# Kernel tuning notes

Hardware: AMD Instinct MI355X
Metric: run time of the kernel (lower is better)

Reference implementation:

```python
import jax, jax.numpy as jnp
import numpy as np

N_NODES = 100000
N_EDGES = 1600000
D_IN = 128
D_HID = 128
D_OUT = 64


def setup_inputs() -> dict:
    key = jax.random.key(0)
    ks = jax.random.split(key, 8)
    x = jax.random.normal(ks[0], (N_NODES, D_IN), dtype=jnp.float32)
    edge_index = jax.random.randint(ks[1], (2, N_EDGES), 0, N_NODES, dtype=jnp.int64)
    s = 1.0 / np.sqrt(D_IN)
    W1l = jax.random.uniform(ks[2], (D_IN, D_HID), minval=-s, maxval=s, dtype=jnp.float32)
    W1r = jax.random.uniform(ks[3], (D_IN, D_HID), minval=-s, maxval=s, dtype=jnp.float32)
    b1 = jnp.zeros((D_HID,), dtype=jnp.float32)
    s2 = 1.0 / np.sqrt(D_HID)
    W2l = jax.random.uniform(ks[4], (D_HID, D_OUT), minval=-s2, maxval=s2, dtype=jnp.float32)
    W2r = jax.random.uniform(ks[5], (D_HID, D_OUT), minval=-s2, maxval=s2, dtype=jnp.float32)
    b2 = jnp.zeros((D_OUT,), dtype=jnp.float32)
    return {"x": x, "edge_index": edge_index, "drpt": 0,
            "W1l": W1l, "W1r": W1r, "b1": b1,
            "W2l": W2l, "W2r": W2r, "b2": b2}


def _mean_aggregate(x, src, dst, n_nodes):
    # gather source features along edges, scatter-mean to destinations
    gathered = x[src]                                   # [E, d]
    summed = jax.ops.segment_sum(gathered, dst, num_segments=n_nodes)  # [N, d]
    deg = jax.ops.segment_sum(jnp.ones((src.shape[0],), x.dtype), dst,
                              num_segments=n_nodes)     # [N]
    return summed / jnp.maximum(deg, 1.0)[:, None]


def _sage_conv(x, src, dst, Wl, Wr, b):
    # PyG SAGEConv (mean): out = agg @ Wl + b + x @ Wr
    agg = _mean_aggregate(x, src, dst, x.shape[0])
    return agg @ Wl + b + x @ Wr


def reference(x, edge_index, drpt, W1l, W1r, b1, W2l, W2r, b2):
    src, dst = edge_index[0], edge_index[1]
    h = _sage_conv(x, src, dst, W1l, W1r, b1)
    h = jax.nn.relu(h)
    # dropout is identity at inference (training=False)
    out = _sage_conv(h, src, dst, W2l, W2r, b2)
    return out
```

## Files before the change

kernel.cpp:

```cpp
#include <hip/hip_runtime.h>
#include <hip/hip_bf16.h>


#define N_NODES 100000
#define NGRP 6250
#define NBKT 391
#define ECHUNK 8192
#define BCAP 12288
#define NXB 12500
#define NWB 192

typedef __attribute__((ext_vector_type(8))) short short8v;
typedef __attribute__((ext_vector_type(4))) float f32x4;
typedef __attribute__((ext_vector_type(2))) uint u32x2;

__device__ inline ushort bf16_rne(float f) {
    union { float f; uint u; } c; c.f = f;
    uint u = c.u;
    return (ushort)((u + 0x7FFFu + ((u >> 16) & 1u)) >> 16);
}
__device__ inline float bf16_f(ushort h) {
    union { uint u; float f; } c; c.u = (uint)h << 16;
    return c.f;
}
__device__ inline unsigned char fp8_enc(float f) {
    union { float f; uint u; } c; c.f = f;
    uint u = c.u;
    uint s = (u >> 24) & 0x80u;
    uint a = u & 0x7FFFFFFFu;
    uint code;
    if (a >= 0x3C800000u) {
        uint r = a + 0x7FFFFu + ((a >> 20) & 1u);
        int e = (int)(r >> 23) - 120;
        uint mm = (r >> 20) & 7u;
        code = ((uint)e << 3) | mm;
        if (code > 0x7Eu) code = 0x7Eu;
    } else {
        code = (uint)(__uint_as_float(a) * 512.0f + 0.5f);
    }
    return (unsigned char)(s | code);
}

__device__ inline void gl_lds16(const void* g, void* l) {
    __builtin_amdgcn_global_load_lds(
        (const __attribute__((address_space(1))) uint*)g,
        (__attribute__((address_space(3))) uint*)l, 16, 0, 0);
}
__device__ inline uint lds_off(const void* p) {
    return (uint)(size_t)(const __attribute__((address_space(3))) char*)p;
}

__global__ __launch_bounds__(256) void k_prep(const float* __restrict__ x,
                                              const float* __restrict__ W1l,
                                              const float* __restrict__ W1r,
                                              const float* __restrict__ W2l,
                                              const float* __restrict__ W2r,
                                              const int* __restrict__ dst, int E,
                                              ushort* __restrict__ xh,
                                              unsigned char* __restrict__ xf8,
                                              ushort* __restrict__ BT1h,
                                              ushort* __restrict__ BT1l,
                                              ushort* __restrict__ BT2h,
                                              ushort* __restrict__ BT2l,
                                              int* __restrict__ bhist) {
    __shared__ int hsh[NBKT];
    const int b = blockIdx.x;
    if (b < NXB) {
        int i = (b * 256 + threadIdx.x) * 4;
        float4 v = *(const float4*)&x[i];
        ushort4 hh;
        hh.x = bf16_rne(v.x); hh.y = bf16_rne(v.y);
        hh.z = bf16_rne(v.z); hh.w = bf16_rne(v.w);
        *(ushort4*)&xh[i] = hh;
        uint f8 = (uint)fp8_enc(v.x) | ((uint)fp8_enc(v.y) << 8) |
                  ((uint)fp8_enc(v.z) << 16) | ((uint)fp8_enc(v.w) << 24);
        *(uint*)&xf8[i] = f8;
    } else if (b < NXB + NWB) {
        int id = (b - NXB) * 256 + threadIdx.x;
        if (id < 32768) {
            int n = id >> 8, k = id & 255;
            float v = (k < 128) ? W1l[k * 128 + n] : W1r[(k - 128) * 128 + n];
            ushort h = bf16_rne(v);
            BT1h[id] = h;
            BT1l[id] = bf16_rne(v - bf16_f(h));
        } else {
            int i = id - 32768;
            int n = i >> 7, k = i & 127;
            float v = (n < 64) ? W2l[k * 64 + n] : W2r[k * 64 + (n - 64)];
            ushort h = bf16_rne(v);
            BT2h[i] = h;
            BT2l[i] = bf16_rne(v - bf16_f(h));
        }
    } else {
        int bb = b - NXB - NWB;
        for (int i = threadIdx.x; i < NBKT; i += 256) hsh[i] = 0;
        __syncthreads();
        int b0 = bb * ECHUNK;
        for (int i = threadIdx.x; i < ECHUNK; i += 256) {
            int e = b0 + i;
            if (e < E) atomicAdd(&hsh[dst[e] >> 8], 1);
        }
        __syncthreads();
        for (int i = threadIdx.x; i < NBKT; i += 256)
            if (hsh[i]) atomicAdd(&bhist[i], hsh[i]);
    }
}

__global__ __launch_bounds__(512) void kA2_scan(const int* __restrict__ bhist,
                                                int* __restrict__ boff,
                                                int* __restrict__ bcur) {
    __shared__ int s[512];
    int t = threadIdx.x;
    s[t] = (t < NBKT) ? bhist[t] : 0;
    __syncthreads();
    for (int d = 1; d < 512; d <<= 1) {
        int v = (t >= d) ? s[t - d] : 0;
        __syncthreads();
        s[t] += v;
        __syncthreads();
    }
    if (t <= NBKT) {
        int e = (t == 0) ? 0 : s[t - 1];
        boff[t] = e;
        if (t < NBKT) bcur[t] = e;
    }
}

__global__ __launch_bounds__(256) void kA3_scatter(const int* __restrict__ src,
                                                   const int* __restrict__ dst,
                                                   int* __restrict__ bcur,
                                                   int* __restrict__ pairs, int E) {
    __shared__ int hist[NBKT];
    __shared__ int base[NBKT];
    __shared__ ushort rank[ECHUNK];
    for (int i = threadIdx.x; i < NBKT; i += 256) hist[i] = 0;
    __syncthreads();
    int b0 = blockIdx.x * ECHUNK;
    for (int i = threadIdx.x; i < ECHUNK; i += 256) {
        int e = b0 + i;
        if (e < E) rank[i] = (ushort)atomicAdd(&hist[dst[e] >> 8], 1);
    }
    __syncthreads();
    for (int i = threadIdx.x; i < NBKT; i += 256) {
        int c = hist[i];
        base[i] = c ? atomicAdd(&bcur[i], c) : 0;
    }
    __syncthreads();
    for (int i = threadIdx.x; i < ECHUNK; i += 256) {
        int e = b0 + i;
        if (e < E) {
            int d = dst[e];
            pairs[base[d >> 8] + rank[i]] = src[e] | ((d & 255) << 17);
        }
    }
}

__global__ __launch_bounds__(256) void kB_build(const int* __restrict__ pairs,
                                                const int* __restrict__ boff,
                                                int* __restrict__ csr,
                                                unsigned char* __restrict__ ldst,
                                                int* __restrict__ offsets,
                                                float* __restrict__ invdeg,
                                                int N, int E) {
    __shared__ int cntk[256];
    __shared__ int sck[256];
    __shared__ int cur[256];
    __shared__ int cntn[256];
    __shared__ int stage[BCAP];
    const int b = blockIdx.x;
    const int gbase = boff[b], gcount = boff[b + 1] - gbase;
    const int n0 = b << 8;
    const int t = threadIdx.x;

    cntk[t] = 0; cntn[t] = 0;
    __syncthreads();
    for (int i = t; i < gcount; i += 256) {
        int p = pairs[gbase + i];
        int dlow = (p >> 17) & 255;
        int key = (dlow & 0xF0) | ((p & 0x1FFFF) >> 13);
        atomicAdd(&cntk[key], 1);
        atomicAdd(&cntn[dlow], 1);
    }
    __syncthreads();
    sck[t] = cntk[t];
    __syncthreads();
    for (int d = 1; d < 256; d <<= 1) {
        int v = (t >= d) ? sck[t - d] : 0;
        __syncthreads();
        sck[t] += v;
        __syncthreads();
    }
    cur[t] = sck[t] - cntk[t];
    int node = n0 + t;
    if (node < N) {
        int gk = t & 0xF0;
        offsets[node] = gbase + sck[gk] - cntk[gk];
        invdeg[node] = 1.0f / fmaxf((float)cntn[t], 1.0f);
    }
    if (b == NBKT - 1 && t == 0) offsets[N] = E;
    __syncthreads();

    if (gcount <= BCAP) {
        for (int i = t; i < gcount; i += 256) {
            int p = pairs[gbase + i];
            int key = ((p >> 17) & 0xF0) | ((p & 0x1FFFF) >> 13);
            int pos = atomicAdd(&cur[key], 1);
            stage[pos] = p;
        }
        __syncthreads();
        for (int i = t; i < gcount; i += 256) {
            int p = stage[i];
            csr[gbase + i] = p & 0x1FFFF;
            ldst[gbase + i] = (unsigned char)((p >> 17) & 15);
        }
    } else {
        for (int i = t; i < gcount; i += 256) {
            int p = pairs[gbase + i];
            int key = ((p >> 17) & 0xF0) | ((p & 0x1FFFF) >> 13);
            int pos = atomicAdd(&cur[key], 1);
            csr[gbase + pos] = p & 0x1FFFF;
            ldst[gbase + pos] = (unsigned char)((p >> 17) & 15);
        }
    }
}

__global__ __launch_bounds__(64, 8) void k_agg1(const unsigned char* __restrict__ xf8,
                                                const int* __restrict__ csr,
                                                const unsigned char* __restrict__ ldst,
                                                const int* __restrict__ off,
                                                const float* __restrict__ invdeg,
                                                ushort* __restrict__ ah, int E) {
    __shared__ __align__(1024) char stg[4096];
    const int lane = threadIdx.x;
    const int g = blockIdx.x;
    const int gbase = off[g * 16], gend = off[g * 16 + 16];
    const int cnt = gend - gbase;
    const int m = lane & 15;
    const int e_meta = lane & 31;
    const int Emax = E - 1;
    const int esrc = lane >> 3;
    const int koff = ((lane & 7) ^ (esrc & 7)) << 4;

    f32x4 acc[8] = {};
    const int nch = (cnt + 31) >> 5;

    int pe = gbase + e_meta;
    int se = csr[(pe < Emax) ? pe : Emax];
    int lb = (pe < gend) ? (int)ldst[pe] : 255;

    const uint e7 = (lane >> 1) & 7;
    const uint bbase = lds_off(stg) + (uint)((lane >> 1) * 128 + (lane & 1) * 8);

    for (int ch = 0; ch < nch; ++ch) {
        #pragma unroll
        for (int c = 0; c < 4; ++c) {
            int rs = __shfl(se, c * 8 + esrc);
            gl_lds16((const char*)xf8 + (size_t)rs * 128 + koff, stg + c * 1024);
        }

        int p = gbase + (ch + 1) * 32 + e_meta;
        se = csr[(p < Emax) ? p : Emax];
        int lbn = (p < gend) ? (int)ldst[p] : 255;

        asm volatile("s_waitcnt vmcnt(0)" ::: "memory");
        __builtin_amdgcn_sched_barrier(0);

        unsigned long long av = 0ull;
        #pragma unroll
        for (int j = 0; j < 8; ++j) {
            int k = (lane >> 4) * 8 + j;
            int b = __shfl(lb, k);
            av |= (b == m) ? (0x38ull << (8 * j)) : 0ull;
        }

        #pragma unroll
        for (int th = 0; th < 2; ++th) {
            u32x2 tb[4];
            #pragma unroll
            for (int t4 = 0; t4 < 4; ++t4) {
                uint t = (uint)(th * 4 + t4);
                uint a1 = bbase + ((t ^ e7) << 4);
                asm volatile("ds_read_b64_tr_b8 %0, %1" : "=v"(tb[t4]) : "v"(a1));
            }
            asm volatile("s_waitcnt lgkmcnt(0)" ::: "memory");
            __builtin_amdgcn_sched_barrier(0);
            #pragma unroll
            for (int t4 = 0; t4 < 4; ++t4) {
                unsigned long long bv = ((unsigned long long)tb[t4].y << 32) | tb[t4].x;
                acc[th * 4 + t4] = __builtin_amdgcn_mfma_f32_16x16x32_fp8_fp8(
                    (long long)av, (long long)bv, acc[th * 4 + t4], 0, 0, 0);
            }
            __builtin_amdgcn_sched_barrier(0);
        }
        lb = lbn;
    }

    float idv[4];
    #pragma unroll
    for (int i = 0; i < 4; ++i) idv[i] = invdeg[g * 16 + (lane >> 4) * 4 + i];
    #pragma unroll
    for (int t = 0; t < 8; ++t) {
        #pragma unroll
        for (int i = 0; i < 4; ++i) {
            int node = g * 16 + (lane >> 4) * 4 + i;
            ah[(size_t)node * 128 + t * 16 + m] = bf16_rne(acc[t][i] * idv[i]);
        }
    }
}

__global__ __launch_bounds__(64, 8) void k_agg2(const ushort* __restrict__ hWl,
                                                const float* __restrict__ hWr,
                                                const int* __restrict__ csr,
                                                const unsigned char* __restrict__ ldst,
                                                const int* __restrict__ off,
                                                const float* __restrict__ invdeg,
                                                const float* __restrict__ b2,
                                                float* __restrict__ out, int E) {
    __shared__ __align__(1024) char stg[4096];
    const int lane = threadIdx.x;
    const int g = blockIdx.x;
    const int gbase = off[g * 16], gend = off[g * 16 + 16];
    const int cnt = gend - gbase;
    const int m = lane & 15;
    const int e_meta = lane & 31;
    const int Emax = E - 1;
    const int esrc = lane >> 3;
    const int koff = ((lane & 7) ^ ((esrc & 3) << 1)) << 4;

    f32x4 acc[4] = {};
    const int nch = (cnt + 31) >> 5;

    int pe = gbase + e_meta;
    int se = csr[(pe < Emax) ? pe : Emax];
    int lb = (pe < gend) ? (int)ldst[pe] : 255;

    const uint he = ((lane >> 1) & 1) ^ (((lane >> 2) & 3) << 1);
    const uint bbase = lds_off(stg) +
        (uint)(((lane >> 4) * 8 + ((lane >> 2) & 3)) * 128 + (lane & 1) * 8);

    for (int ch = 0; ch < nch; ++ch) {
        #pragma unroll
        for (int c = 0; c < 4; ++c) {
            int rs = __shfl(se, c * 8 + esrc);
            gl_lds16((const char*)hWl + (size_t)rs * 128 + koff, stg + c * 1024);
        }

        int p = gbase + (ch + 1) * 32 + e_meta;
        se = csr[(p < Emax) ? p : Emax];
        int lbn = (p < gend) ? (int)ldst[p] : 255;

        asm volatile("s_waitcnt vmcnt(0)" ::: "memory");
        __builtin_amdgcn_sched_barrier(0);

        uint au[4];
        #pragma unroll
        for (int jp = 0; jp < 4; ++jp) {
            int k0 = (lane >> 4) * 8 + jp * 2;
            int b0 = __shfl(lb, k0);
            int b1 = __shfl(lb, k0 + 1);
            au[jp] = ((b0 == m) ? 0x3F80u : 0u) | (((b1 == m) ? 0x3F80u : 0u) << 16);
        }
        union { uint u[4]; short8v v; } A_;
        A_.u[0] = au[0]; A_.u[1] = au[1]; A_.u[2] = au[2]; A_.u[3] = au[3];

        #pragma unroll
        for (int th = 0; th < 2; ++th) {
            u32x2 t1[2], t2[2];
            #pragma unroll
            for (int tt = 0; tt < 2; ++tt) {
                uint t = (uint)(th * 2 + tt);
                uint seg = (2u * t) ^ he;
                uint a1 = bbase + (seg << 4);
                uint a2 = a1 + 512;
                asm volatile("ds_read_b64_tr_b16 %0, %1" : "=v"(t1[tt]) : "v"(a1));
                asm volatile("ds_read_b64_tr_b16 %0, %1" : "=v"(t2[tt]) : "v"(a2));
            }
            asm volatile("s_waitcnt lgkmcnt(0)" ::: "memory");
            __builtin_amdgcn_sched_barrier(0);
            #pragma unroll
            for (int tt = 0; tt < 2; ++tt) {
                union { uint u[4]; short8v v; } B_;
                B_.u[0] = t1[tt].x; B_.u[1] = t1[tt].y;
                B_.u[2] = t2[tt].x; B_.u[3] = t2[tt].y;
                acc[th * 2 + tt] = __builtin_amdgcn_mfma_f32_16x16x32_bf16(
                    A_.v, B_.v, acc[th * 2 + tt], 0, 0, 0);
            }
            __builtin_amdgcn_sched_barrier(0);
        }
        lb = lbn;
    }

    float idv[4];
    #pragma unroll
    for (int i = 0; i < 4; ++i) idv[i] = invdeg[g * 16 + (lane >> 4) * 4 + i];
    #pragma unroll
    for (int t = 0; t < 4; ++t) {
        #pragma unroll
        for (int i = 0; i < 4; ++i) {
            int node = g * 16 + (lane >> 4) * 4 + i;
            size_t idx = (size_t)node * 64 + t * 16 + m;
            out[idx] = acc[t][i] * idv[i] + hWr[idx] + b2[t * 16 + m];
        }
    }
}

__global__ __launch_bounds__(256, 3) void k_mfma12(
    const ushort* __restrict__ Agg, const ushort* __restrict__ X,
    const ushort* __restrict__ B1h, const ushort* __restrict__ B1l,
    const ushort* __restrict__ B2h, const ushort* __restrict__ B2l,
    const float* __restrict__ b1,
    ushort* __restrict__ hWl, float* __restrict__ hWr, int M) {
    __shared__ ushort SM[24576];
    ushort* Bh  = SM;
    ushort* Bl  = SM + 4096;
    ushort* AhT = SM + 8192;

    const int tid = threadIdx.x;
    const int wid = tid >> 6, lane = tid & 63;
    const int wm = wid >> 1, wn = wid & 1;
    const int m0 = blockIdx.x * 128;
    const int rl = lane & 15, kq = lane >> 4;
    const int rq = kq;

    const int r0 = tid >> 2, r1 = r0 + 64;
    const int cq = tid & 3;
    int g0 = m0 + r0; if (g0 >= M) g0 = M - 1;
    int g1 = m0 + r1; if (g1 >= M) g1 = M - 1;
    const int q0 = (cq ^ ((r0 >> 1) & 3)) * 8;
    const int q1 = (cq ^ ((r1 >> 1) & 3)) * 8;
    const int ldso0 = r0 * 32 + cq * 8;
    const int ldso1 = r1 * 32 + cq * 8;

    int aof[4], bof[4];
    #pragma unroll
    for (int f = 0; f < 4; ++f) {
        int ra = wm * 64 + f * 16 + rl;
        int rb = wn * 64 + f * 16 + rl;
        aof[f] = ra * 32 + ((kq ^ ((ra >> 1) & 3)) << 3);
        bof[f] = rb * 32 + ((kq ^ ((rb >> 1) & 3)) << 3);
    }

    short8v pA0, pA1, pB0, pB1, pL0, pL1;
    {
        pA0 = *(const short8v*)&Agg[(size_t)g0 * 128 + q0];
        pA1 = *(const short8v*)&Agg[(size_t)g1 * 128 + q1];
        pB0 = *(const short8v*)&B1h[r0 * 256 + q0];
        pB1 = *(const short8v*)&B1h[r1 * 256 + q1];
        pL0 = *(const short8v*)&B1l[r0 * 256 + q0];
        pL1 = *(const short8v*)&B1l[r1 * 256 + q1];
    }
    f32x4 acc[4][4] = {};
    for (int kc = 0; kc < 8; ++kc) {
        *(short8v*)&AhT[ldso0] = pA0; *(short8v*)&AhT[ldso1] = pA1;
        *(short8v*)&Bh[ldso0]  = pB0; *(short8v*)&Bh[ldso1]  = pB1;
        *(short8v*)&Bl[ldso0]  = pL0; *(short8v*)&Bl[ldso1]  = pL1;
        __syncthreads();

        if (kc < 7) {
            int gk0 = (kc + 1) * 32 + q0;
            int gk1 = (kc + 1) * 32 + q1;
            const ushort* s0 = (kc + 1 >= 4) ? &X[(size_t)g0 * 128 + gk0 - 128]
                                             : &Agg[(size_t)g0 * 128 + gk0];
            const ushort* s1 = (kc + 1 >= 4) ? &X[(size_t)g1 * 128 + gk1 - 128]
                                             : &Agg[(size_t)g1 * 128 + gk1];
            pA0 = *(const short8v*)s0;
            pA1 = *(const short8v*)s1;
            pB0 = *(const short8v*)&B1h[r0 * 256 + gk0];
            pB1 = *(const short8v*)&B1h[r1 * 256 + gk1];
            pL0 = *(const short8v*)&B1l[r0 * 256 + gk0];
            pL1 = *(const short8v*)&B1l[r1 * 256 + gk1];
        }

        short8v a_h[4], b_h[4], b_l[4];
        #pragma unroll
        for (int f = 0; f < 4; ++f) {
            a_h[f] = *(const short8v*)&AhT[aof[f]];
            b_h[f] = *(const short8v*)&Bh[bof[f]];
            b_l[f] = *(const short8v*)&Bl[bof[f]];
        }
        #pragma unroll
        for (int mf = 0; mf < 4; ++mf)
            #pragma unroll
            for (int nf = 0; nf < 4; ++nf) {
                acc[mf][nf] = __builtin_amdgcn_mfma_f32_16x16x32_bf16(a_h[mf], b_h[nf], acc[mf][nf], 0, 0, 0);
                acc[mf][nf] = __builtin_amdgcn_mfma_f32_16x16x32_bf16(a_h[mf], b_l[nf], acc[mf][nf], 0, 0, 0);
            }
        __syncthreads();
    }

    short8v qB0, qB1, qL0, qL1;
    {
        qB0 = *(const short8v*)&B2h[r0 * 128 + q0];
        qB1 = *(const short8v*)&B2h[r1 * 128 + q1];
        qL0 = *(const short8v*)&B2l[r0 * 128 + q0];
        qL1 = *(const short8v*)&B2l[r1 * 128 + q1];
    }

    #pragma unroll
    for (int mf = 0; mf < 4; ++mf)
        #pragma unroll
        for (int nf = 0; nf < 4; ++nf) {
            int col = wn * 64 + nf * 16 + rl;
            float bv = b1[col];
            int cc = col >> 5;
            int ic = col & 31;
            int gq = ic >> 3;
            #pragma unroll
            for (int i = 0; i < 4; ++i) {
                int rloc = wm * 64 + mf * 16 + rq * 4 + i;
                float v = fmaxf(acc[mf][nf][i] + bv, 0.0f);
                int rho = cc * 128 + rloc;
                AhT[rho * 32 + ((gq ^ ((rloc >> 1) & 3)) << 3) + (ic & 7)] = bf16_rne(v);
            }
        }
    __syncthreads();

    f32x4 acc2[4][4] = {};
    for (int kc = 0; kc < 4; ++kc) {
        *(short8v*)&Bh[ldso0] = qB0; *(short8v*)&Bh[ldso1] = qB1;
        *(short8v*)&Bl[ldso0] = qL0; *(short8v*)&Bl[ldso1] = qL1;
        __syncthreads();

        if (kc < 3) {
            int gk0 = (kc + 1) * 32 + q0;
            int gk1 = (kc + 1) * 32 + q1;
            qB0 = *(const short8v*)&B2h[r0 * 128 + gk0];
            qB1 = *(const short8v*)&B2h[r1 * 128 + gk1];
            qL0 = *(const short8v*)&B2l[r0 * 128 + gk0];
            qL1 = *(const short8v*)&B2l[r1 * 128 + gk1];
        }

        short8v a_h[4], b_h[4], b_l[4];
        #pragma unroll
        for (int f = 0; f < 4; ++f) {
            a_h[f] = *(const short8v*)&AhT[kc * 4096 + aof[f]];
            b_h[f] = *(const short8v*)&Bh[bof[f]];
            b_l[f] = *(const short8v*)&Bl[bof[f]];
        }
        #pragma unroll
        for (int mf = 0; mf < 4; ++mf)
            #pragma unroll
            for (int nf = 0; nf < 4; ++nf) {
                acc2[mf][nf] = __builtin_amdgcn_mfma_f32_16x16x32_bf16(a_h[mf], b_h[nf], acc2[mf][nf], 0, 0, 0);
                acc2[mf][nf] = __builtin_amdgcn_mfma_f32_16x16x32_bf16(a_h[mf], b_l[nf], acc2[mf][nf], 0, 0, 0);
            }
        __syncthreads();
    }

    #pragma unroll
    for (int mf = 0; mf < 4; ++mf)
        #pragma unroll
        for (int nf = 0; nf < 4; ++nf) {
            int col = wn * 64 + nf * 16 + rl;
            #pragma unroll
            for (int i = 0; i < 4; ++i) {
                int row = m0 + wm * 64 + mf * 16 + rq * 4 + i;
                if (row < M) {
                    float v = acc2[mf][nf][i];
                    if (col < 64) hWl[(size_t)row * 64 + col] = bf16_rne(v);
                    else          hWr[(size_t)row * 64 + col - 64] = v;
                }
            }
        }
}

extern "C" void kernel_launch(void* const* d_in, const int* in_sizes, int n_in,
                              void* d_out, int out_size, void* d_ws, size_t ws_size,
                              hipStream_t stream) {
    const float* x   = (const float*)d_in[0];
    const int*   ei  = (const int*)d_in[1];
    const float* W1l = (const float*)d_in[3];
    const float* W1r = (const float*)d_in[4];
    const float* b1  = (const float*)d_in[5];
    const float* W2l = (const float*)d_in[6];
    const float* W2r = (const float*)d_in[7];
    const float* b2  = (const float*)d_in[8];
    float* out = (float*)d_out;

    const int N = N_NODES;
    const int E = in_sizes[1] / 2;
    const int* src = ei;
    const int* dst = ei + E;
    const int NEB = (E + ECHUNK - 1) / ECHUNK;

    char* ws = (char*)d_ws;
    int*           bhist   = (int*)   (ws + 0);
    int*           boff    = (int*)   (ws + 4096);
    int*           bcur    = (int*)   (ws + 8192);
    int*           offsets = (int*)   (ws + 12288);
    float*         invdeg  = (float*) (ws + 417792);
    int*           csr     = (int*)   (ws + 819200);
    unsigned char* ldst    = (unsigned char*)(ws + 7220224);
    unsigned char* x_f8    = (unsigned char*)(ws + 8821760);
    ushort*        x_hi    = (ushort*)(ws + 21622784);
    ushort*        agg_hi  = (ushort*)(ws + 47223808);
    float*         hWr     = (float*) (ws + 98425856);
    ushort*        BT1h    = (ushort*)(ws + 124026880);
    ushort*        BT1l    = (ushort*)(ws + 124092416);
    ushort*        BT2h    = (ushort*)(ws + 124157952);
    ushort*        BT2l    = (ushort*)(ws + 124190720);
    int*           pairs   = (int*)   (ws + 98425856);
    ushort*        hWl     = (ushort*)(ws + 72824832);

    hipMemsetAsync(bhist, 0, NBKT * 4, stream);

    k_prep<<<NXB + NWB + NEB, 256, 0, stream>>>(x, W1l, W1r, W2l, W2r, dst, E,
                                                x_hi, x_f8, BT1h, BT1l, BT2h, BT2l, bhist);
    kA2_scan<<<1, 512, 0, stream>>>(bhist, boff, bcur);
    kA3_scatter<<<NEB, 256, 0, stream>>>(src, dst, bcur, pairs, E);
    kB_build<<<NBKT, 256, 0, stream>>>(pairs, boff, csr, ldst, offsets, invdeg, N, E);

    k_agg1<<<NGRP, 64, 0, stream>>>(x_f8, csr, ldst, offsets, invdeg, agg_hi, E);

    const int MB = (N + 127) / 128;
    k_mfma12<<<MB, 256, 0, stream>>>(agg_hi, x_hi, BT1h, BT1l, BT2h, BT2l,
                                     b1, hWl, hWr, N);

    k_agg2<<<NGRP, 64, 0, stream>>>(hWl, hWr, csr, ldst, offsets, invdeg, b2, out, E);
}
```

Baseline: 171.8 us.

## Double-buffer LDS staging of gathered rows in both aggregation kernels

Both aggregation kernels now use two 4KB LDS staging buffers. Each iteration issues the gather of the next 32-edge chunk into the alternate buffer before running the MFMAs on the current one, and waits with partial vmcnt counts instead of draining all outstanding loads. This hides gather latency behind compute, at the cost of doubled shared memory and reliance on exact vmcnt accounting across csr/ldst prefetch loads.

```diff
diff --git a/kernel.cpp b/kernel.cpp
--- a/kernel.cpp
+++ b/kernel.cpp
@@ -230,7 +230,7 @@
                                                 const int* __restrict__ off,
                                                 const float* __restrict__ invdeg,
                                                 ushort* __restrict__ ah, int E) {
-    __shared__ __align__(1024) char stg[4096];
+    __shared__ __align__(1024) char stg[8192];
     const int lane = threadIdx.x;
     const int g = blockIdx.x;
     const int gbase = off[g * 16], gend = off[g * 16 + 16];
@@ -244,32 +244,49 @@
     f32x4 acc[8] = {};
     const int nch = (cnt + 31) >> 5;
 
-    int pe = gbase + e_meta;
-    int se = csr[(pe < Emax) ? pe : Emax];
-    int lb = (pe < gend) ? (int)ldst[pe] : 255;
+    int p0 = gbase + e_meta;
+    int se_cur = csr[(p0 < Emax) ? p0 : Emax];
+    int lb_cur = (p0 < gend) ? (int)ldst[p0] : 255;
+    int p1 = p0 + 32;
+    int se_nxt = csr[(p1 < Emax) ? p1 : Emax];
+    int lb_nxt = (p1 < gend) ? (int)ldst[p1] : 255;
+
+    {
+        #pragma unroll
+        for (int c = 0; c < 4; ++c) {
+            int rs = __shfl(se_cur, c * 8 + esrc);
+            gl_lds16((const char*)xf8 + (size_t)rs * 128 + koff, stg + c * 1024);
+        }
+    }
 
     const uint e7 = (lane >> 1) & 7;
-    const uint bbase = lds_off(stg) + (uint)((lane >> 1) * 128 + (lane & 1) * 8);
+    const uint bbase0 = lds_off(stg) + (uint)((lane >> 1) * 128 + (lane & 1) * 8);
 
     for (int ch = 0; ch < nch; ++ch) {
-        #pragma unroll
-        for (int c = 0; c < 4; ++c) {
-            int rs = __shfl(se, c * 8 + esrc);
-            gl_lds16((const char*)xf8 + (size_t)rs * 128 + koff, stg + c * 1024);
-        }
-
-        int p = gbase + (ch + 1) * 32 + e_meta;
-        se = csr[(p < Emax) ? p : Emax];
-        int lbn = (p < gend) ? (int)ldst[p] : 255;
-
-        asm volatile("s_waitcnt vmcnt(0)" ::: "memory");
+        char* nxtb = stg + ((ch & 1) ? 0 : 4096);
+        uint bbase = bbase0 + ((ch & 1) ? 4096u : 0u);
+
+        int p2 = gbase + (ch + 2) * 32 + e_meta;
+        int se2 = csr[(p2 < Emax) ? p2 : Emax];
+        int lb2 = (p2 < gend) ? (int)ldst[p2] : 255;
+        __builtin_amdgcn_sched_barrier(0);
+        if (ch + 1 < nch) {
+            #pragma unroll
+            for (int c = 0; c < 4; ++c) {
+                int rs = __shfl(se_nxt, c * 8 + esrc);
+                gl_lds16((const char*)xf8 + (size_t)rs * 128 + koff, nxtb + c * 1024);
+            }
+            asm volatile("s_waitcnt vmcnt(6)" ::: "memory");
+        } else {
+            asm volatile("s_waitcnt vmcnt(2)" ::: "memory");
+        }
         __builtin_amdgcn_sched_barrier(0);
 
         unsigned long long av = 0ull;
         #pragma unroll
         for (int j = 0; j < 8; ++j) {
             int k = (lane >> 4) * 8 + j;
-            int b = __shfl(lb, k);
+            int b = __shfl(lb_cur, k);
             av |= (b == m) ? (0x38ull << (8 * j)) : 0ull;
         }
 
@@ -292,7 +309,7 @@
             }
             __builtin_amdgcn_sched_barrier(0);
         }
-        lb = lbn;
+        se_nxt = se2; lb_cur = lb_nxt; lb_nxt = lb2;
     }
 
     float idv[4];
@@ -316,7 +333,7 @@
                                                 const float* __restrict__ invdeg,
                                                 const float* __restrict__ b2,
                                                 float* __restrict__ out, int E) {
-    __shared__ __align__(1024) char stg[4096];
+    __shared__ __align__(1024) char stg[8192];
     const int lane = threadIdx.x;
     const int g = blockIdx.x;
     const int gbase = off[g * 16], gend = off[g * 16 + 16];
@@ -330,34 +347,51 @@
     f32x4 acc[4] = {};
     const int nch = (cnt + 31) >> 5;
 
-    int pe = gbase + e_meta;
-    int se = csr[(pe < Emax) ? pe : Emax];
-    int lb = (pe < gend) ? (int)ldst[pe] : 255;
+    int p0 = gbase + e_meta;
+    int se_cur = csr[(p0 < Emax) ? p0 : Emax];
+    int lb_cur = (p0 < gend) ? (int)ldst[p0] : 255;
+    int p1 = p0 + 32;
+    int se_nxt = csr[(p1 < Emax) ? p1 : Emax];
+    int lb_nxt = (p1 < gend) ? (int)ldst[p1] : 255;
+
+    {
+        #pragma unroll
+        for (int c = 0; c < 4; ++c) {
+            int rs = __shfl(se_cur, c * 8 + esrc);
+            gl_lds16((const char*)hWl + (size_t)rs * 128 + koff, stg + c * 1024);
+        }
+    }
 
     const uint he = ((lane >> 1) & 1) ^ (((lane >> 2) & 3) << 1);
-    const uint bbase = lds_off(stg) +
+    const uint bbase0 = lds_off(stg) +
         (uint)(((lane >> 4) * 8 + ((lane >> 2) & 3)) * 128 + (lane & 1) * 8);
 
     for (int ch = 0; ch < nch; ++ch) {
-        #pragma unroll
-        for (int c = 0; c < 4; ++c) {
-            int rs = __shfl(se, c * 8 + esrc);
-            gl_lds16((const char*)hWl + (size_t)rs * 128 + koff, stg + c * 1024);
-        }
-
-        int p = gbase + (ch + 1) * 32 + e_meta;
-        se = csr[(p < Emax) ? p : Emax];
-        int lbn = (p < gend) ? (int)ldst[p] : 255;
-
-        asm volatile("s_waitcnt vmcnt(0)" ::: "memory");
+        char* nxtb = stg + ((ch & 1) ? 0 : 4096);
+        uint bbase = bbase0 + ((ch & 1) ? 4096u : 0u);
+
+        int p2 = gbase + (ch + 2) * 32 + e_meta;
+        int se2 = csr[(p2 < Emax) ? p2 : Emax];
+        int lb2 = (p2 < gend) ? (int)ldst[p2] : 255;
+        __builtin_amdgcn_sched_barrier(0);
+        if (ch + 1 < nch) {
+            #pragma unroll
+            for (int c = 0; c < 4; ++c) {
+                int rs = __shfl(se_nxt, c * 8 + esrc);
+                gl_lds16((const char*)hWl + (size_t)rs * 128 + koff, nxtb + c * 1024);
+            }
+            asm volatile("s_waitcnt vmcnt(6)" ::: "memory");
+        } else {
+            asm volatile("s_waitcnt vmcnt(2)" ::: "memory");
+        }
         __builtin_amdgcn_sched_barrier(0);
 
         uint au[4];
         #pragma unroll
         for (int jp = 0; jp < 4; ++jp) {
             int k0 = (lane >> 4) * 8 + jp * 2;
-            int b0 = __shfl(lb, k0);
-            int b1 = __shfl(lb, k0 + 1);
+            int b0 = __shfl(lb_cur, k0);
+            int b1 = __shfl(lb_cur, k0 + 1);
             au[jp] = ((b0 == m) ? 0x3F80u : 0u) | (((b1 == m) ? 0x3F80u : 0u) << 16);
         }
         union { uint u[4]; short8v v; } A_;
@@ -387,7 +421,7 @@
             }
             __builtin_amdgcn_sched_barrier(0);
         }
-        lb = lbn;
+        se_nxt = se2; lb_cur = lb_nxt; lb_nxt = lb2;
     }
 
     float idv[4];
```

After: 180.2 us. 1.05x slower.

## Drop low-part split of layer-2 weights and issue prefetch loads before barrier

Applied to the files above, without the earlier changes.

The second GEMM now uses only the bf16 high part of W2, which halves its MFMA count and drops the low-part LDS stores and loads along with the extra global reads. Both GEMM loops now issue the next tile's global loads into temporaries before the barrier, with a sched_barrier so the loads stay ahead of the sync and overlap with the MFMA work. In exchange, layer-2 accuracy falls to plain bf16 weight precision, and keeping the prefetch temporaries live may raise register pressure.

```diff
diff --git a/kernel.cpp b/kernel.cpp
--- a/kernel.cpp
+++ b/kernel.cpp
@@ -61,7 +61,6 @@
                                               ushort* __restrict__ BT1h,
                                               ushort* __restrict__ BT1l,
                                               ushort* __restrict__ BT2h,
-                                              ushort* __restrict__ BT2l,
                                               int* __restrict__ bhist) {
     __shared__ int hsh[NBKT];
     const int b = blockIdx.x;
@@ -87,9 +86,7 @@
             int i = id - 32768;
             int n = i >> 7, k = i & 127;
             float v = (n < 64) ? W2l[k * 64 + n] : W2r[k * 64 + (n - 64)];
-            ushort h = bf16_rne(v);
-            BT2h[i] = h;
-            BT2l[i] = bf16_rne(v - bf16_f(h));
+            BT2h[i] = bf16_rne(v);
         }
     } else {
         int bb = b - NXB - NWB;
@@ -407,7 +404,7 @@
 __global__ __launch_bounds__(256, 3) void k_mfma12(
     const ushort* __restrict__ Agg, const ushort* __restrict__ X,
     const ushort* __restrict__ B1h, const ushort* __restrict__ B1l,
-    const ushort* __restrict__ B2h, const ushort* __restrict__ B2l,
+    const ushort* __restrict__ B2h,
     const float* __restrict__ b1,
     ushort* __restrict__ hWl, float* __restrict__ hWr, int M) {
     __shared__ ushort SM[24576];
@@ -454,8 +451,8 @@
         *(short8v*)&AhT[ldso0] = pA0; *(short8v*)&AhT[ldso1] = pA1;
         *(short8v*)&Bh[ldso0]  = pB0; *(short8v*)&Bh[ldso1]  = pB1;
         *(short8v*)&Bl[ldso0]  = pL0; *(short8v*)&Bl[ldso1]  = pL1;
-        __syncthreads();
-
+
+        short8v nA0, nA1, nB0, nB1, nL0, nL1;
         if (kc < 7) {
             int gk0 = (kc + 1) * 32 + q0;
             int gk1 = (kc + 1) * 32 + q1;
@@ -463,13 +460,17 @@
                                              : &Agg[(size_t)g0 * 128 + gk0];
             const ushort* s1 = (kc + 1 >= 4) ? &X[(size_t)g1 * 128 + gk1 - 128]
                                              : &Agg[(size_t)g1 * 128 + gk1];
-            pA0 = *(const short8v*)s0;
-            pA1 = *(const short8v*)s1;
-            pB0 = *(const short8v*)&B1h[r0 * 256 + gk0];
-            pB1 = *(const short8v*)&B1h[r1 * 256 + gk1];
-            pL0 = *(const short8v*)&B1l[r0 * 256 + gk0];
-            pL1 = *(const short8v*)&B1l[r1 * 256 + gk1];
-        }
+            nA0 = *(const short8v*)s0;
+            nA1 = *(const short8v*)s1;
+            nB0 = *(const short8v*)&B1h[r0 * 256 + gk0];
+            nB1 = *(const short8v*)&B1h[r1 * 256 + gk1];
+            nL0 = *(const short8v*)&B1l[r0 * 256 + gk0];
+            nL1 = *(const short8v*)&B1l[r1 * 256 + gk1];
+        } else {
+            nA0 = pA0; nA1 = pA1; nB0 = pB0; nB1 = pB1; nL0 = pL0; nL1 = pL1;
+        }
+        __builtin_amdgcn_sched_barrier(0);
+        __syncthreads();
 
         short8v a_h[4], b_h[4], b_l[4];
         #pragma unroll
@@ -486,14 +487,13 @@
                 acc[mf][nf] = __builtin_amdgcn_mfma_f32_16x16x32_bf16(a_h[mf], b_l[nf], acc[mf][nf], 0, 0, 0);
             }
         __syncthreads();
-    }
-
-    short8v qB0, qB1, qL0, qL1;
+        pA0 = nA0; pA1 = nA1; pB0 = nB0; pB1 = nB1; pL0 = nL0; pL1 = nL1;
+    }
+
+    short8v qB0, qB1;
     {
         qB0 = *(const short8v*)&B2h[r0 * 128 + q0];
         qB1 = *(const short8v*)&B2h[r1 * 128 + q1];
-        qL0 = *(const short8v*)&B2l[r0 * 128 + q0];
-        qL1 = *(const short8v*)&B2l[r1 * 128 + q1];
     }
 
     #pragma unroll
@@ -518,33 +518,33 @@
     f32x4 acc2[4][4] = {};
     for (int kc = 0; kc < 4; ++kc) {
         *(short8v*)&Bh[ldso0] = qB0; *(short8v*)&Bh[ldso1] = qB1;
-        *(short8v*)&Bl[ldso0] = qL0; *(short8v*)&Bl[ldso1] = qL1;
-        __syncthreads();
-
+
+        short8v nB0, nB1;
         if (kc < 3) {
             int gk0 = (kc + 1) * 32 + q0;
             int gk1 = (kc + 1) * 32 + q1;
-            qB0 = *(const short8v*)&B2h[r0 * 128 + gk0];
-            qB1 = *(const short8v*)&B2h[r1 * 128 + gk1];
-            qL0 = *(const short8v*)&B2l[r0 * 128 + gk0];
-            qL1 = *(const short8v*)&B2l[r1 * 128 + gk1];
-        }
-
-        short8v a_h[4], b_h[4], b_l[4];
+            nB0 = *(const short8v*)&B2h[r0 * 128 + gk0];
+            nB1 = *(const short8v*)&B2h[r1 * 128 + gk1];
+        } else {
+            nB0 = qB0; nB1 = qB1;
+        }
+        __builtin_amdgcn_sched_barrier(0);
+        __syncthreads();
+
+        short8v a_h[4], b_h[4];
         #pragma unroll
         for (int f = 0; f < 4; ++f) {
             a_h[f] = *(const short8v*)&AhT[kc * 4096 + aof[f]];
             b_h[f] = *(const short8v*)&Bh[bof[f]];
-            b_l[f] = *(const short8v*)&Bl[bof[f]];
         }
         #pragma unroll
         for (int mf = 0; mf < 4; ++mf)
             #pragma unroll
             for (int nf = 0; nf < 4; ++nf) {
                 acc2[mf][nf] = __builtin_amdgcn_mfma_f32_16x16x32_bf16(a_h[mf], b_h[nf], acc2[mf][nf], 0, 0, 0);
-                acc2[mf][nf] = __builtin_amdgcn_mfma_f32_16x16x32_bf16(a_h[mf], b_l[nf], acc2[mf][nf], 0, 0, 0);
-            }
-        __syncthreads();
+            }
+        __syncthreads();
+        qB0 = nB0; qB1 = nB1;
     }
 
     #pragma unroll
@@ -598,14 +598,13 @@
     ushort*        BT1h    = (ushort*)(ws + 124026880);
     ushort*        BT1l    = (ushort*)(ws + 124092416);
     ushort*        BT2h    = (ushort*)(ws + 124157952);
-    ushort*        BT2l    = (ushort*)(ws + 124190720);
     int*           pairs   = (int*)   (ws + 98425856);
     ushort*        hWl     = (ushort*)(ws + 72824832);
 
     hipMemsetAsync(bhist, 0, NBKT * 4, stream);
 
     k_prep<<<NXB + NWB + NEB, 256, 0, stream>>>(x, W1l, W1r, W2l, W2r, dst, E,
-                                                x_hi, x_f8, BT1h, BT1l, BT2h, BT2l, bhist);
+                                                x_hi, x_f8, BT1h, BT1l, BT2h, bhist);
     kA2_scan<<<1, 512, 0, stream>>>(bhist, boff, bcur);
     kA3_scatter<<<NEB, 256, 0, stream>>>(src, dst, bcur, pairs, E);
     kB_build<<<NBKT, 256, 0, stream>>>(pairs, boff, csr, ldst, offsets, invdeg, N, E);
@@ -613,7 +612,7 @@
     k_agg1<<<NGRP, 64, 0, stream>>>(x_f8, csr, ldst, offsets, invdeg, agg_hi, E);
 
     const int MB = (N + 127) / 128;
-    k_mfma12<<<MB, 256, 0, stream>>>(agg_hi, x_hi, BT1h, BT1l, BT2h, BT2l,
+    k_mfma12<<<MB, 256, 0, stream>>>(agg_hi, x_hi, BT1h, BT1l, BT2h,
                                      b1, hWl, hWr, N);
 
     k_agg2<<<NGRP, 64, 0, stream>>>(hWl, hWr, csr, ldst, offsets, invdeg, b2, out, E);
```

Result: faster. 167.4 us, median of 2 (-2.5%).
